# Kernel optimization log

Hardware: AMD Instinct MI355X
Metric: run time of the kernel (lower is better)

The kernel has to match this reference:

```python
import jax, jax.numpy as jnp
import numpy as np


def setup_inputs() -> dict:
    key = jax.random.key(0)
    k1, k2 = jax.random.split(key, 2)
    N, H, W, FIN = 64, 64, 64, 64
    FH, FW, FOUT = 4, 4, 128
    L = (H // FH) * (W // FW)  # 256 output locations (stride == kernel)
    X = jax.random.normal(k1, (N, H, W, FIN), dtype=jnp.float32)
    # 'alexnet' init: normal(0, 0.01), unshared per-location filters
    filters = 0.01 * jax.random.normal(k2, (1, L, FH, FW, FIN, FOUT), dtype=jnp.float32)
    bias = jnp.zeros((FOUT,), dtype=jnp.float32)  # bias init value 0.0
    return {"X": X, "filters": filters, "bias": bias}


def reference(X, filters, bias):
    N, H, W, C = X.shape
    _, L, fh, fw, fin, fout = filters.shape
    rows, cols = H // fh, W // fw
    # image_to_patches (stride==kernel branch): non-overlapping patch extraction
    # patches[n, r*cols+c, i, j, ch] = X[n, r*fh+i, c*fw+j, ch]
    patches = X.reshape(N, rows, fh, cols, fw, C)
    patches = patches.transpose(0, 1, 3, 2, 4, 5).reshape(N, L, fh, fw, C)
    # broadcast-multiply + reduce_sum over (fh, fw, fin) == per-location GEMM
    Z = jnp.einsum('nlijc,lijcf->nlf', patches, filters[0]) + bias
    Z = Z.reshape(N, rows, cols, fout)
    return jax.nn.relu(Z)
```

## Files before the change

kernel.cpp:

```cpp
#include <hip/hip_runtime.h>


typedef __bf16 bf16x8 __attribute__((ext_vector_type(8)));
typedef float f32x4 __attribute__((ext_vector_type(4)));

#define SBQ 36

__device__ __forceinline__ unsigned pack2(float a, float b) {
  __bf16 lo = (__bf16)a, hi = (__bf16)b;
  return (unsigned)__builtin_bit_cast(unsigned short, lo) |
         ((unsigned)__builtin_bit_cast(unsigned short, hi) << 16);
}
__device__ __forceinline__ bf16x8 cvt8(float4 lo, float4 hi) {
  uint4 v;
  v.x = pack2(lo.x, lo.y);
  v.y = pack2(lo.z, lo.w);
  v.z = pack2(hi.x, hi.y);
  v.w = pack2(hi.z, hi.w);
  return __builtin_bit_cast(bf16x8, v);
}

__global__ __launch_bounds__(64) void bioconv_wave(
    const float* __restrict__ X, const float* __restrict__ Fw,
    const float* __restrict__ bias, float* __restrict__ out) {
  const int bx = blockIdx.x;
  const int l = bx & 255;
  const int fq = bx >> 8;
  const int r = l >> 4, c = l & 15;
  const int lane = threadIdx.x;
  const int q = lane >> 4, nl = lane & 15;

  __shared__ __align__(16) unsigned Bs[2][16 * SBQ];

  const float* pA[4];
#pragma unroll
  for (int mb = 0; mb < 4; ++mb)
    pA[mb] = X + (size_t)(mb * 16 + nl) * 262144 + r * 16384 + c * 256 + q * 8;

  const float* pB = Fw + (size_t)l * 131072 + fq * 32 + (lane >> 3) * 256 + (lane & 7) * 4;
  unsigned* const wpB = (unsigned*)Bs + ((lane >> 3) * SBQ + (lane & 7) * 4);

  float4 aR[2][8];
  float4 bR[3][4];
  f32x4 acc[4][2];
#pragma unroll
  for (int mb = 0; mb < 4; ++mb) {
    acc[mb][0] = (f32x4){0.f, 0.f, 0.f, 0.f};
    acc[mb][1] = (f32x4){0.f, 0.f, 0.f, 0.f};
  }

  auto issueA = [&](int s, int ring) {
    const int p = s >> 1;
    const int off = (p >> 2) * 4096 + (p & 3) * 64 + (s & 1) * 32;
#pragma unroll
    for (int mb = 0; mb < 4; ++mb) {
      aR[ring][mb * 2] = *(const float4*)(pA[mb] + off);
      aR[ring][mb * 2 + 1] = *(const float4*)(pA[mb] + off + 4);
    }
  };
  auto issueB = [&](int s, int ring) {
#pragma unroll
    for (int rep = 0; rep < 2; ++rep) {
      const float* g = pB + s * 4096 + rep * 2048;
      bR[ring][rep * 2] = *(const float4*)(g);
      bR[ring][rep * 2 + 1] = *(const float4*)(g + 128);
    }
  };
  auto writeB = [&](int s, int ring) {
    unsigned* wp = wpB + (s & 1) * (16 * SBQ);
#pragma unroll
    for (int rep = 0; rep < 2; ++rep) {
      float4 e0 = bR[ring][rep * 2], e1 = bR[ring][rep * 2 + 1];
      uint4 v;
      v.x = pack2(e0.x, e1.x);
      v.y = pack2(e0.y, e1.y);
      v.z = pack2(e0.z, e1.z);
      v.w = pack2(e0.w, e1.w);
      *(uint4*)(wp + rep * 8 * SBQ) = v;
    }
  };

  issueA(0, 0);
  issueB(0, 0);
  issueA(1, 1);
  issueB(1, 1);
  issueB(2, 2);
  writeB(0, 0);

#pragma unroll
  for (int s = 0; s < 32; ++s) {
    if (s + 3 < 32) issueB(s + 3, (s + 3) % 3);
    if (s + 1 < 32) writeB(s + 1, (s + 1) % 3);

    bf16x8 af[4];
#pragma unroll
    for (int mb = 0; mb < 4; ++mb)
      af[mb] = cvt8(aR[s & 1][mb * 2], aR[s & 1][mb * 2 + 1]);
    if (s + 2 < 32) issueA(s + 2, s & 1);

#pragma unroll
    for (int fb = 0; fb < 2; ++fb) {
      const unsigned* bp = &Bs[s & 1][(q * 4) * SBQ + fb * 16 + nl];
      uint4 v;
      v.x = bp[0];
      v.y = bp[SBQ];
      v.z = bp[2 * SBQ];
      v.w = bp[3 * SBQ];
      bf16x8 bfr = __builtin_bit_cast(bf16x8, v);
#pragma unroll
      for (int mb = 0; mb < 4; ++mb)
        acc[mb][fb] = __builtin_amdgcn_mfma_f32_16x16x32_bf16(af[mb], bfr, acc[mb][fb], 0, 0, 0);
    }
  }

#pragma unroll
  for (int fb = 0; fb < 2; ++fb) {
    const int f = fq * 32 + fb * 16 + nl;
    const float bv = bias[f];
    float* ob = out + (size_t)l * 128 + f;
#pragma unroll
    for (int mb = 0; mb < 4; ++mb) {
#pragma unroll
      for (int v = 0; v < 4; ++v) {
        const int row = mb * 16 + q * 4 + v;
        ob[(size_t)row * 32768] = fmaxf(acc[mb][fb][v] + bv, 0.f);
      }
    }
  }
}

extern "C" void kernel_launch(void* const* d_in, const int* in_sizes, int n_in,
                              void* d_out, int out_size, void* d_ws, size_t ws_size,
                              hipStream_t stream) {
  const float* X = (const float*)d_in[0];
  const float* Fw = (const float*)d_in[1];
  const float* bias = (const float*)d_in[2];
  float* out = (float*)d_out;
  bioconv_wave<<<1024, 64, 0, stream>>>(X, Fw, bias, out);
}
```

Measured before the change: 240.4 us.

## Split batch rows across four waves per block with XCD-aware block mapping

Each 64-row block now runs four waves, and each wave computes one 16-row M-slice instead of one wave computing all four. This raises the number of resident waves and cuts the register footprint per wave, so more memory latency can be hidden. Block indices are remapped so that the blocks sharing one location land on the same XCD, which should improve L2 reuse of the filter tiles. As a cost, each wave loads and converts its own copy of the B tile into a private LDS buffer, so filter traffic into L1/L2 and LDS use both grow fourfold.

Result: slower. 252.3 us (+5.0%).

```diff
diff --git a/kernel.cpp b/kernel.cpp
--- a/kernel.cpp
+++ b/kernel.cpp
@@ -20,43 +20,39 @@
   return __builtin_bit_cast(bf16x8, v);
 }
 
-__global__ __launch_bounds__(64) void bioconv_wave(
+__global__ __launch_bounds__(256, 4) void bioconv_wave4(
     const float* __restrict__ X, const float* __restrict__ Fw,
     const float* __restrict__ bias, float* __restrict__ out) {
   const int bx = blockIdx.x;
-  const int l = bx & 255;
-  const int fq = bx >> 8;
+  const int xcd = bx & 7;
+  const int idx = bx >> 3;
+  const int l = xcd * 32 + (idx >> 2);
+  const int fq = idx & 3;
   const int r = l >> 4, c = l & 15;
-  const int lane = threadIdx.x;
+  const int tid = threadIdx.x;
+  const int wave = tid >> 6;
+  const int lane = tid & 63;
   const int q = lane >> 4, nl = lane & 15;
 
-  __shared__ __align__(16) unsigned Bs[2][16 * SBQ];
+  __shared__ __align__(16) unsigned Bs[4][2][16 * SBQ];
 
-  const float* pA[4];
-#pragma unroll
-  for (int mb = 0; mb < 4; ++mb)
-    pA[mb] = X + (size_t)(mb * 16 + nl) * 262144 + r * 16384 + c * 256 + q * 8;
+  const float* pA =
+      X + (size_t)(wave * 16 + nl) * 262144 + r * 16384 + c * 256 + q * 8;
 
   const float* pB = Fw + (size_t)l * 131072 + fq * 32 + (lane >> 3) * 256 + (lane & 7) * 4;
-  unsigned* const wpB = (unsigned*)Bs + ((lane >> 3) * SBQ + (lane & 7) * 4);
+  unsigned* const wpB = (unsigned*)Bs[wave] + ((lane >> 3) * SBQ + (lane & 7) * 4);
 
-  float4 aR[2][8];
+  float4 aR[2][2];
   float4 bR[3][4];
-  f32x4 acc[4][2];
-#pragma unroll
-  for (int mb = 0; mb < 4; ++mb) {
-    acc[mb][0] = (f32x4){0.f, 0.f, 0.f, 0.f};
-    acc[mb][1] = (f32x4){0.f, 0.f, 0.f, 0.f};
-  }
+  f32x4 acc[2];
+  acc[0] = (f32x4){0.f, 0.f, 0.f, 0.f};
+  acc[1] = (f32x4){0.f, 0.f, 0.f, 0.f};
 
   auto issueA = [&](int s, int ring) {
     const int p = s >> 1;
     const int off = (p >> 2) * 4096 + (p & 3) * 64 + (s & 1) * 32;
-#pragma unroll
-    for (int mb = 0; mb < 4; ++mb) {
-      aR[ring][mb * 2] = *(const float4*)(pA[mb] + off);
-      aR[ring][mb * 2 + 1] = *(const float4*)(pA[mb] + off + 4);
-    }
+    aR[ring][0] = *(const float4*)(pA + off);
+    aR[ring][1] = *(const float4*)(pA + off + 4);
   };
   auto issueB = [&](int s, int ring) {
 #pragma unroll
@@ -92,24 +88,19 @@
     if (s + 3 < 32) issueB(s + 3, (s + 3) % 3);
     if (s + 1 < 32) writeB(s + 1, (s + 1) % 3);
 
-    bf16x8 af[4];
-#pragma unroll
-    for (int mb = 0; mb < 4; ++mb)
-      af[mb] = cvt8(aR[s & 1][mb * 2], aR[s & 1][mb * 2 + 1]);
+    bf16x8 af = cvt8(aR[s & 1][0], aR[s & 1][1]);
     if (s + 2 < 32) issueA(s + 2, s & 1);
 
 #pragma unroll
     for (int fb = 0; fb < 2; ++fb) {
-      const unsigned* bp = &Bs[s & 1][(q * 4) * SBQ + fb * 16 + nl];
+      const unsigned* bp = &Bs[wave][s & 1][(q * 4) * SBQ + fb * 16 + nl];
       uint4 v;
       v.x = bp[0];
       v.y = bp[SBQ];
       v.z = bp[2 * SBQ];
       v.w = bp[3 * SBQ];
       bf16x8 bfr = __builtin_bit_cast(bf16x8, v);
-#pragma unroll
-      for (int mb = 0; mb < 4; ++mb)
-        acc[mb][fb] = __builtin_amdgcn_mfma_f32_16x16x32_bf16(af[mb], bfr, acc[mb][fb], 0, 0, 0);
+      acc[fb] = __builtin_amdgcn_mfma_f32_16x16x32_bf16(af, bfr, acc[fb], 0, 0, 0);
     }
   }
 
@@ -119,12 +110,9 @@
     const float bv = bias[f];
     float* ob = out + (size_t)l * 128 + f;
 #pragma unroll
-    for (int mb = 0; mb < 4; ++mb) {
-#pragma unroll
-      for (int v = 0; v < 4; ++v) {
-        const int row = mb * 16 + q * 4 + v;
-        ob[(size_t)row * 32768] = fmaxf(acc[mb][fb][v] + bv, 0.f);
-      }
+    for (int v = 0; v < 4; ++v) {
+      const int row = wave * 16 + q * 4 + v;
+      ob[(size_t)row * 32768] = fmaxf(acc[fb][v] + bv, 0.f);
     }
   }
 }
@@ -136,5 +124,5 @@
   const float* Fw = (const float*)d_in[1];
   const float* bias = (const float*)d_in[2];
   float* out = (float*)d_out;
-  bioconv_wave<<<1024, 64, 0, stream>>>(X, Fw, bias, out);
+  bioconv_wave4<<<1024, 256, 0, stream>>>(X, Fw, bias, out);
 }
```
